# Performance work log

Hardware: AMD Instinct MI355X
Metric: run time of the kernel (lower is better)

## Reference

```python
import jax, jax.numpy as jnp
import numpy as np

K = 7          # kernel_size (odd)
STRIDE = 1
PAD = K // 2
SIGMA_GUIDE = 1.0


def _unfold6(x, k, stride, pad):
    """torch F.unfold equivalent -> (bs, ch, k, k, oh, ow)."""
    bs, ch = x.shape[:2]
    patches = jax.lax.conv_general_dilated_patches(
        x, filter_shape=(k, k), window_strides=(stride, stride),
        padding=[(pad, pad), (pad, pad)])  # (bs, ch*k*k, oh, ow), channel-major
    oh, ow = patches.shape[2:]
    return patches.reshape(bs, ch, k, k, oh, ow)


def setup_inputs() -> dict:
    key = jax.random.key(0)
    k1, k2 = jax.random.split(key, 2)
    input = jax.random.normal(k1, (2, 32, 256, 256), dtype=jnp.float32)
    input_for_kernel = jax.random.normal(k2, (2, 3, 256, 256), dtype=jnp.float32)
    sigma_for_kernel = jnp.asarray(float(K) / 4.0, dtype=jnp.float32)  # Parameter init
    return {"input": input, "input_for_kernel": input_for_kernel,
            "sigma_for_kernel": sigma_for_kernel}


def reference(input, input_for_kernel, sigma_for_kernel):
    dt = input.dtype
    # spatial Gaussian kernel (truncated, normalized)
    r = jnp.arange(-(K // 2), K // 2 + 1, dtype=dt)
    g1 = jnp.exp(-0.5 * r * r / (sigma_for_kernel * sigma_for_kernel))
    g2 = g1[:, None] * g1[None, :]
    g2 = g2 / g2.sum()  # (K, K)

    # data-dependent range (guide) kernel: GaussKernel2dFn, channel_wise=False
    g = input_for_kernel / SIGMA_GUIDE                      # (b, cg, H, W)
    cols_g = _unfold6(g, K, STRIDE, PAD)                    # (b, cg, K, K, H, W)
    diff = cols_g - g[:, :, None, None]                     # center = window middle (stride 1)
    guide = jnp.exp(-0.5 * jnp.sum(diff * diff, axis=1, keepdims=True))  # (b,1,K,K,H,W)

    ker = g2[None, None, :, :, None, None] * guide          # (b,1,K,K,H,W)
    norm = ker.sum(axis=(2, 3), keepdims=True)
    ker = ker / (norm + (norm == 0).astype(dt))

    # ApplyKernelFn: unfold input, multiply by per-pixel kernel, sum over window
    in_cols = _unfold6(input, K, STRIDE, PAD)               # (b, c, K, K, H, W)
    out = jnp.einsum('bcklhw,bzklhw->bchw', in_cols, ker)
    return out
```

## Files before the change

### kernel.cpp

```cpp
#include <hip/hip_runtime.h>

#define KS    7
#define RAD   3
#define TW    32
#define TH    8
#define HR    14
#define PAIRS 21
#define NSITE (HR*2*PAIRS)
#define H     256
#define W     256
#define HWp   (H*W)
#define NTASK (HR*10*4)

typedef __fp16    h2raw __attribute__((ext_vector_type(2)));
typedef _Float16  f16x2 __attribute__((ext_vector_type(2)));

__device__ __forceinline__ unsigned pk(float a, float b) {
    h2raw h = __builtin_amdgcn_cvt_pkrtz(a, b);
    return __builtin_bit_cast(unsigned, h);
}
__device__ __forceinline__ f16x2 bch(unsigned u) {
    return __builtin_bit_cast(f16x2, u);
}

#if __has_builtin(__builtin_amdgcn_fdot2)
__device__ __forceinline__ float fdot2(f16x2 a, f16x2 b, float c) {
    return __builtin_amdgcn_fdot2(a, b, c, false);
}
#else
__device__ __forceinline__ float fdot2(f16x2 a, f16x2 b, float c) {
    return c + (float)a.x * (float)b.x + (float)a.y * (float)b.y;
}
#endif

#define ISSUE_IN(g) do {                                                    \
    _Pragma("unroll")                                                       \
    for (int j = 0; j < 3; ++j) {                                           \
        int t = tid + j * 256;                                              \
        iA[j] = make_float4(0.f, 0.f, 0.f, 0.f); iB[j] = iA[j];             \
        if (t < NTASK) {                                                    \
            int row = t / 40;                                               \
            int rem = t - row * 40;                                         \
            int q   = rem >> 2;                                             \
            int cp  = rem & 3;                                              \
            int gy  = y0 - RAD + row;                                       \
            int gxb = x0 - 4 + 4 * q;                                       \
            if (gy >= 0 && gy < H && gxb >= 0 && gxb < W) {                 \
                const float* p = inb + (size_t)((g) * 8 + 2 * cp) * HWp     \
                                 + gy * W + gxb;                            \
                iA[j] = *(const float4*)p;                                  \
                iB[j] = *(const float4*)(p + HWp);                          \
            }                                                               \
        }                                                                   \
    }                                                                       \
} while (0)

#define WRITE_IN(g) do {                                                    \
    _Pragma("unroll")                                                       \
    for (int j = 0; j < 3; ++j) {                                           \
        int t = tid + j * 256;                                              \
        if (t < NTASK) {                                                    \
            int row = t / 40;                                               \
            int rem = t - row * 40;                                         \
            int q   = rem >> 2;                                             \
            int cp  = rem & 3;                                              \
            int s0  = row * 2 * PAIRS + 2 * q;                              \
            unsigned* dst = &dtu[(g)][cp];                                  \
            if (q != 0) dst[(s0 + PAIRS - 1) * 4] = pk(iA[j].x, iB[j].x);   \
            dst[s0 * 4]           = pk(iA[j].y, iB[j].y);                   \
            dst[(s0 + PAIRS) * 4] = pk(iA[j].z, iB[j].z);                   \
            if (q != 9) dst[(s0 + 1) * 4] = pk(iA[j].w, iB[j].w);           \
        }                                                                   \
    }                                                                       \
} while (0)

#define APPLY(g) do {                                                       \
    const uint4* dg = (const uint4*)&dtu[(g)][0];                           \
    float acc[8];                                                           \
    _Pragma("unroll") for (int c = 0; c < 8; ++c) acc[c] = 0.f;             \
    _Pragma("unroll")                                                       \
    for (int i = 0; i < KS; ++i) {                                          \
        const int rb = (ty + i) * 2 * PAIRS;                                \
        uint4 rq[KS];                                                       \
        _Pragma("unroll")                                                   \
        for (int k = 0; k < KS; ++k) rq[k] = dg[rb + colAdd[k]];            \
        f16x2 A0 = (f16x2)0, A1 = (f16x2)0, A2 = (f16x2)0, A3 = (f16x2)0;   \
        _Pragma("unroll")                                                   \
        for (int k = 0; k < KS; ++k) {                                      \
            f16x2 wh = bch(wkp[i * KS + k]);                                \
            A0 = wh * bch(rq[k].x) + A0;                                    \
            A1 = wh * bch(rq[k].y) + A1;                                    \
            A2 = wh * bch(rq[k].z) + A2;                                    \
            A3 = wh * bch(rq[k].w) + A3;                                    \
        }                                                                   \
        acc[0] += (float)A0.x; acc[1] += (float)A0.y;                       \
        acc[2] += (float)A1.x; acc[3] += (float)A1.y;                       \
        acc[4] += (float)A2.x; acc[5] += (float)A2.y;                       \
        acc[6] += (float)A3.x; acc[7] += (float)A3.y;                       \
    }                                                                       \
    float* ob = out + ((size_t)b * 32 + (g) * 8) * HWp                      \
                + (size_t)Yo * W + Xo;                                      \
    _Pragma("unroll")                                                       \
    for (int c = 0; c < 8; ++c) ob[(size_t)c * HWp] = acc[c] * inv;         \
} while (0)

__global__ __launch_bounds__(256)
void bilateral_kernel(const float* __restrict__ in,
                      const float* __restrict__ guide,
                      const float* __restrict__ sigma_p,
                      float* __restrict__ out)
{
    __shared__ uint2 gt2[NSITE];
    __shared__ __align__(16) unsigned dtu[4][NSITE * 4];

    const int tid = threadIdx.x;
    const int tx  = tid & 31;
    const int ty  = tid >> 5;
    const int x0  = blockIdx.x * TW;
    const int y0  = blockIdx.y * TH;
    const int b   = blockIdx.z;

    const float* gb  = guide + (size_t)b * 3  * HWp;
    const float* inb = in    + (size_t)b * 32 * HWp;

    const float sigma = sigma_p[0];
    const float isig2 = 1.0f / (sigma * sigma);
    const float L2E   = 1.442695041f;
    const float SQL   = 1.201122409f;
    float lnT2[KS];
#pragma unroll
    for (int i = 0; i < KS; ++i) {
        float r = (float)(i - RAD);
        lnT2[i] = -0.5f * r * r * isig2 * L2E;
    }

    float4 gX = make_float4(0.f, 0.f, 0.f, 0.f), gY = gX, gZ = gX;
    int grow = 0, gq = 0;
    if (tid < HR * 10) {
        grow = tid / 10; gq = tid - grow * 10;
        int gy  = y0 - RAD + grow;
        int gxb = x0 - 4 + 4 * gq;
        if (gy >= 0 && gy < H && gxb >= 0 && gxb < W) {
            const float* p = gb + gy * W + gxb;
            gX = *(const float4*)p;
            gY = *(const float4*)(p + HWp);
            gZ = *(const float4*)(p + 2 * HWp);
        }
    }
    float4 iA[3], iB[3];
    ISSUE_IN(0);

    if (tid < HR * 10) {
        int s0 = grow * 2 * PAIRS + 2 * gq;
        const float xs[4] = {gX.x, gX.y, gX.z, gX.w};
        const float ys[4] = {gY.x, gY.y, gY.z, gY.w};
        const float zs[4] = {gZ.x, gZ.y, gZ.z, gZ.w};
        const int   st[4] = {s0 + PAIRS - 1, s0, s0 + PAIRS, s0 + 1};
#pragma unroll
        for (int j = 0; j < 4; ++j) {
            if ((gq == 0 && j == 0) || (gq == 9 && j == 3)) continue;
            float ax = xs[j] * SQL, ay = ys[j] * SQL, az = zs[j] * SQL;
            float qv = -0.5f * (ax * ax + ay * ay + az * az);
            gt2[st[j]] = make_uint2(pk(ax, ay), pk(az, qv));
        }
    }
    __syncthreads();

    int colAdd[KS];
#pragma unroll
    for (int k = 0; k < KS; ++k) {
        int col = tx + k;
        colAdd[k] = (col & 1) * PAIRS + (col >> 1);
    }

    const int ccol = tx + RAD;
    uint2 cr = gt2[(ty + RAD) * 2 * PAIRS + (ccol & 1) * PAIRS + (ccol >> 1)];
    const f16x2 cxy = bch(cr.x);
    f16x2 czq = bch(cr.y);
    const float qc = (float)czq.y;
    f16x2 cz1;
    cz1.x = czq.x; cz1.y = (_Float16)1.0f;

    unsigned wkp[KS * KS];
    float nsum = 0.f;
#pragma unroll
    for (int i = 0; i < KS; ++i) {
        const int rb = (ty + i) * 2 * PAIRS;
        const float Qi = lnT2[i] + qc;
#pragma unroll
        for (int k = 0; k < KS; ++k) {
            uint2 g = gt2[rb + colAdd[k]];
            float e = fdot2(bch(g.x), cxy, fdot2(bch(g.y), cz1, Qi + lnT2[k]));
            float w = exp2f(e);
            nsum += w;
            wkp[i * KS + k] = pk(w, w);
        }
    }
    const float inv = 1.f / nsum;
    const int Xo = x0 + tx, Yo = y0 + ty;

    WRITE_IN(0);
    __syncthreads();
    ISSUE_IN(1);
    APPLY(0);
    WRITE_IN(1);
    __syncthreads();
    ISSUE_IN(2);
    APPLY(1);
    WRITE_IN(2);
    __syncthreads();
    ISSUE_IN(3);
    APPLY(2);
    WRITE_IN(3);
    __syncthreads();
    APPLY(3);
}

extern "C" void kernel_launch(void* const* d_in, const int* in_sizes, int n_in,
                              void* d_out, int out_size, void* d_ws, size_t ws_size,
                              hipStream_t stream) {
    const float* in    = (const float*)d_in[0];
    const float* guide = (const float*)d_in[1];
    const float* sigma = (const float*)d_in[2];
    float* out = (float*)d_out;
    dim3 grid(W / TW, H / TH, 2);
    bilateral_kernel<<<grid, dim3(256), 0, stream>>>(in, guide, sigma, out);
}
```

Baseline: 22.54 us.

## Use single-wavefront 8x8 tiles and drop block barriers for compiler fences

Shrinks each block from 256 threads on a 32x8 tile to one 64-thread wavefront on an 8x8 tile. Because a block is now a single wavefront, the __syncthreads calls become compiler-only memory fences. The LDS staging drops from four channel-group buffers to two ping-pong buffers, and launch bounds allow three blocks per CU. The aim is to remove barrier stalls and raise occupancy, at the cost of a larger halo per output pixel (14x14 loaded for 64 outputs), so global and L2 traffic and guide-weight recomputation go up.

```diff
diff --git a/kernel.cpp b/kernel.cpp
--- a/kernel.cpp
+++ b/kernel.cpp
@@ -2,15 +2,16 @@
 
 #define KS    7
 #define RAD   3
-#define TW    32
-#define TH    8
+#define TS    8
+#define HC    14
 #define HR    14
-#define PAIRS 21
-#define NSITE (HR*2*PAIRS)
+#define PAIRS 8
+#define ROWST (2*PAIRS)
+#define NSITE (HR*ROWST)
 #define H     256
 #define W     256
 #define HWp   (H*W)
-#define NTASK (HR*10*4)
+#define NTASK (HR*4*4)
 
 typedef __fp16    h2raw __attribute__((ext_vector_type(2)));
 typedef _Float16  f16x2 __attribute__((ext_vector_type(2)));
@@ -33,14 +34,16 @@
 }
 #endif
 
+#define FENCE() asm volatile("" ::: "memory")
+
 #define ISSUE_IN(g) do {                                                    \
     _Pragma("unroll")                                                       \
-    for (int j = 0; j < 3; ++j) {                                           \
-        int t = tid + j * 256;                                              \
+    for (int j = 0; j < 4; ++j) {                                           \
+        int t = tid + j * 64;                                               \
         iA[j] = make_float4(0.f, 0.f, 0.f, 0.f); iB[j] = iA[j];             \
         if (t < NTASK) {                                                    \
-            int row = t / 40;                                               \
-            int rem = t - row * 40;                                         \
+            int row = t >> 4;                                               \
+            int rem = t & 15;                                               \
             int q   = rem >> 2;                                             \
             int cp  = rem & 3;                                              \
             int gy  = y0 - RAD + row;                                       \
@@ -55,32 +58,32 @@
     }                                                                       \
 } while (0)
 
-#define WRITE_IN(g) do {                                                    \
-    _Pragma("unroll")                                                       \
-    for (int j = 0; j < 3; ++j) {                                           \
-        int t = tid + j * 256;                                              \
+#define WRITE_IN(buf) do {                                                  \
+    _Pragma("unroll")                                                       \
+    for (int j = 0; j < 4; ++j) {                                           \
+        int t = tid + j * 64;                                               \
         if (t < NTASK) {                                                    \
-            int row = t / 40;                                               \
-            int rem = t - row * 40;                                         \
+            int row = t >> 4;                                               \
+            int rem = t & 15;                                               \
             int q   = rem >> 2;                                             \
             int cp  = rem & 3;                                              \
-            int s0  = row * 2 * PAIRS + 2 * q;                              \
-            unsigned* dst = &dtu[(g)][cp];                                  \
-            if (q != 0) dst[(s0 + PAIRS - 1) * 4] = pk(iA[j].x, iB[j].x);   \
-            dst[s0 * 4]           = pk(iA[j].y, iB[j].y);                   \
-            dst[(s0 + PAIRS) * 4] = pk(iA[j].z, iB[j].z);                   \
-            if (q != 9) dst[(s0 + 1) * 4] = pk(iA[j].w, iB[j].w);           \
+            int base = row * ROWST;                                         \
+            unsigned* dst = &dtu[(buf)][cp];                                \
+            if (q != 0) dst[(base + PAIRS + 2 * q - 1) * 4] = pk(iA[j].x, iB[j].x); \
+            dst[(base + 2 * q) * 4]         = pk(iA[j].y, iB[j].y);         \
+            dst[(base + PAIRS + 2 * q) * 4] = pk(iA[j].z, iB[j].z);         \
+            if (q != 3) dst[(base + 2 * q + 1) * 4] = pk(iA[j].w, iB[j].w); \
         }                                                                   \
     }                                                                       \
 } while (0)
 
-#define APPLY(g) do {                                                       \
-    const uint4* dg = (const uint4*)&dtu[(g)][0];                           \
+#define APPLY(buf, g) do {                                                  \
+    const uint4* dg = (const uint4*)&dtu[(buf)][0];                         \
     float acc[8];                                                           \
     _Pragma("unroll") for (int c = 0; c < 8; ++c) acc[c] = 0.f;             \
     _Pragma("unroll")                                                       \
     for (int i = 0; i < KS; ++i) {                                          \
-        const int rb = (ty + i) * 2 * PAIRS;                                \
+        const int rb = (ty + i) * ROWST;                                    \
         uint4 rq[KS];                                                       \
         _Pragma("unroll")                                                   \
         for (int k = 0; k < KS; ++k) rq[k] = dg[rb + colAdd[k]];            \
@@ -104,20 +107,20 @@
     for (int c = 0; c < 8; ++c) ob[(size_t)c * HWp] = acc[c] * inv;         \
 } while (0)
 
-__global__ __launch_bounds__(256)
+__global__ __launch_bounds__(64, 3)
 void bilateral_kernel(const float* __restrict__ in,
                       const float* __restrict__ guide,
                       const float* __restrict__ sigma_p,
                       float* __restrict__ out)
 {
     __shared__ uint2 gt2[NSITE];
-    __shared__ __align__(16) unsigned dtu[4][NSITE * 4];
+    __shared__ __align__(16) unsigned dtu[2][NSITE * 4];
 
     const int tid = threadIdx.x;
-    const int tx  = tid & 31;
-    const int ty  = tid >> 5;
-    const int x0  = blockIdx.x * TW;
-    const int y0  = blockIdx.y * TH;
+    const int tx  = tid & 7;
+    const int ty  = tid >> 3;
+    const int x0  = blockIdx.x * TS;
+    const int y0  = blockIdx.y * TS;
     const int b   = blockIdx.z;
 
     const float* gb  = guide + (size_t)b * 3  * HWp;
@@ -136,8 +139,8 @@
 
     float4 gX = make_float4(0.f, 0.f, 0.f, 0.f), gY = gX, gZ = gX;
     int grow = 0, gq = 0;
-    if (tid < HR * 10) {
-        grow = tid / 10; gq = tid - grow * 10;
+    if (tid < HR * 4) {
+        grow = tid >> 2; gq = tid & 3;
         int gy  = y0 - RAD + grow;
         int gxb = x0 - 4 + 4 * gq;
         if (gy >= 0 && gy < H && gxb >= 0 && gxb < W) {
@@ -147,24 +150,25 @@
             gZ = *(const float4*)(p + 2 * HWp);
         }
     }
-    float4 iA[3], iB[3];
+    float4 iA[4], iB[4];
     ISSUE_IN(0);
 
-    if (tid < HR * 10) {
-        int s0 = grow * 2 * PAIRS + 2 * gq;
+    if (tid < HR * 4) {
+        int base = grow * ROWST;
         const float xs[4] = {gX.x, gX.y, gX.z, gX.w};
         const float ys[4] = {gY.x, gY.y, gY.z, gY.w};
         const float zs[4] = {gZ.x, gZ.y, gZ.z, gZ.w};
-        const int   st[4] = {s0 + PAIRS - 1, s0, s0 + PAIRS, s0 + 1};
+        const int   st[4] = {base + PAIRS + 2 * gq - 1, base + 2 * gq,
+                             base + PAIRS + 2 * gq,     base + 2 * gq + 1};
 #pragma unroll
         for (int j = 0; j < 4; ++j) {
-            if ((gq == 0 && j == 0) || (gq == 9 && j == 3)) continue;
+            if ((gq == 0 && j == 0) || (gq == 3 && j == 3)) continue;
             float ax = xs[j] * SQL, ay = ys[j] * SQL, az = zs[j] * SQL;
             float qv = -0.5f * (ax * ax + ay * ay + az * az);
             gt2[st[j]] = make_uint2(pk(ax, ay), pk(az, qv));
         }
     }
-    __syncthreads();
+    FENCE();
 
     int colAdd[KS];
 #pragma unroll
@@ -174,7 +178,7 @@
     }
 
     const int ccol = tx + RAD;
-    uint2 cr = gt2[(ty + RAD) * 2 * PAIRS + (ccol & 1) * PAIRS + (ccol >> 1)];
+    uint2 cr = gt2[(ty + RAD) * ROWST + (ccol & 1) * PAIRS + (ccol >> 1)];
     const f16x2 cxy = bch(cr.x);
     f16x2 czq = bch(cr.y);
     const float qc = (float)czq.y;
@@ -185,7 +189,7 @@
     float nsum = 0.f;
 #pragma unroll
     for (int i = 0; i < KS; ++i) {
-        const int rb = (ty + i) * 2 * PAIRS;
+        const int rb = (ty + i) * ROWST;
         const float Qi = lnT2[i] + qc;
 #pragma unroll
         for (int k = 0; k < KS; ++k) {
@@ -200,20 +204,20 @@
     const int Xo = x0 + tx, Yo = y0 + ty;
 
     WRITE_IN(0);
-    __syncthreads();
+    FENCE();
     ISSUE_IN(1);
-    APPLY(0);
+    APPLY(0, 0);
     WRITE_IN(1);
-    __syncthreads();
+    FENCE();
     ISSUE_IN(2);
-    APPLY(1);
-    WRITE_IN(2);
-    __syncthreads();
+    APPLY(1, 1);
+    WRITE_IN(0);
+    FENCE();
     ISSUE_IN(3);
-    APPLY(2);
-    WRITE_IN(3);
-    __syncthreads();
-    APPLY(3);
+    APPLY(0, 2);
+    WRITE_IN(1);
+    FENCE();
+    APPLY(1, 3);
 }
 
 extern "C" void kernel_launch(void* const* d_in, const int* in_sizes, int n_in,
@@ -223,6 +227,6 @@
     const float* guide = (const float*)d_in[1];
     const float* sigma = (const float*)d_in[2];
     float* out = (float*)d_out;
-    dim3 grid(W / TW, H / TH, 2);
-    bilateral_kernel<<<grid, dim3(256), 0, stream>>>(in, guide, sigma, out);
-}
+    dim3 grid(W / TS, H / TS, 2);
+    bilateral_kernel<<<grid, dim3(64), 0, stream>>>(in, guide, sigma, out);
+}
```

Result: slower. 42.37 us (+87.9%).
